# Performance work log

Hardware: AMD Instinct MI355X
Metric: run time of the kernel (lower is better)

The kernel has to match this reference:

```python
import jax, jax.numpy as jnp
import numpy as np

EPS = 1e-5

def _bn_relu(z, gamma, beta):
    # BatchNorm1d (training mode: biased batch stats) + ReLU, per-feature over batch dim
    mean = jnp.mean(z, axis=0)
    var = jnp.var(z, axis=0)  # biased, matches torch BN normalization
    zn = (z - mean) * jax.lax.rsqrt(var + EPS) * gamma + beta
    return jax.nn.relu(zn)


def setup_inputs() -> dict:
    key = jax.random.key(0)
    ks = jax.random.split(key, 16)
    N, D_IN, H, D_OUT = 2097152, 16, 32, 1
    def lin(kw, kb, fan_in, fan_out):
        bound = 1.0 / np.sqrt(fan_in)
        W = jax.random.uniform(kw, (fan_out, fan_in), jnp.float32, -bound, bound)
        b = jax.random.uniform(kb, (fan_out,), jnp.float32, -bound, bound)
        return W, b
    W1, b1 = lin(ks[0], ks[1], D_IN, H)
    W2, b2 = lin(ks[2], ks[3], H, H)
    W3, b3 = lin(ks[4], ks[5], H, H)
    W4, b4 = lin(ks[6], ks[7], H, D_OUT)
    x = jax.random.normal(ks[8], (N, D_IN), jnp.float32)
    return {
        "x": x,
        "W1": W1, "b1": b1, "g1": jnp.ones((H,), jnp.float32), "be1": jnp.zeros((H,), jnp.float32),
        "W2": W2, "b2": b2, "g2": jnp.ones((H,), jnp.float32), "be2": jnp.zeros((H,), jnp.float32),
        "W3": W3, "b3": b3, "g3": jnp.ones((H,), jnp.float32), "be3": jnp.zeros((H,), jnp.float32),
        "W4": W4, "b4": b4,
    }


def reference(x, W1, b1, g1, be1, W2, b2, g2, be2, W3, b3, g3, be3, W4, b4):
    p1 = _bn_relu(x @ W1.T + b1, g1, be1)    # [N, H]
    p2 = _bn_relu(p1 @ W2.T + b2, g2, be2)   # [N, H]
    p3 = _bn_relu(p2 @ W3.T + b3, g3, be3)   # [N, H]
    return p3 @ W4.T + b4                    # [N, 1]
```

## Files before the change

kernel.cpp:

```cpp
#include <hip/hip_runtime.h>

#define EPS 1e-5f
#define NTHR 256
#define NBLK 1024
#define NSLOT 64

typedef __bf16 bf16x8 __attribute__((ext_vector_type(8)));
typedef float f32x16 __attribute__((ext_vector_type(16)));


template<int DEPTH>
__global__ __launch_bounds__(NTHR) void k_fwd(
    const float* __restrict__ x, __bf16* __restrict__ xb,
    const float* __restrict__ W1, const float* __restrict__ b1,
    const float* __restrict__ g1, const float* __restrict__ be1,
    const float* __restrict__ W2, const float* __restrict__ b2,
    const float* __restrict__ g2, const float* __restrict__ be2,
    const float* __restrict__ W3, const float* __restrict__ b3,
    const float* __restrict__ g3, const float* __restrict__ be3,
    const float* __restrict__ W4, const float* __restrict__ b4,
    float* __restrict__ stats, float* __restrict__ out, int N)
{
    constexpr bool STATS = (DEPTH < 4);
    __shared__ float s_stat[3][64];
    __shared__ float s_a[3][32];
    __shared__ float s_e[3][32];
    __shared__ float s_w[NTHR / 64][64];

    const int tid = threadIdx.x;
    const float invN = 1.0f / (float)N;

    if (tid < 64) {
        for (int L = 0; L < DEPTH - 1; ++L) {
            float a = 0.f;
            #pragma unroll 8
            for (int s = 0; s < NSLOT; ++s) a += stats[L * (NSLOT * 64) + s * 64 + tid];
            s_stat[L][tid] = a;
        }
    }
    __syncthreads();
    if (tid < 32) {
        const float* gs[3]  = {g1, g2, g3};
        const float* bes[3] = {be1, be2, be3};
        const float* bs[3]  = {b1, b2, b3};
        for (int L = 0; L < DEPTH - 1; ++L) {
            float mu = s_stat[L][tid] * invN;
            float v  = s_stat[L][32 + tid] * invN - mu * mu;
            float a  = gs[L][tid] * rsqrtf(v + EPS);
            s_a[L][tid] = a;
            s_e[L][tid] = bs[L][tid] - mu + bes[L][tid] / a;
        }
    }
    __syncthreads();

    const int lane = tid & 63;
    const int h = lane >> 5;
    const int ml = lane & 31;

    bf16x8 w1f;
    {
        const float* p = W1 + ml * 16 + h * 8;
        #pragma unroll
        for (int j = 0; j < 8; ++j) w1f[j] = (__bf16)p[j];
    }
    bf16x8 w2f0 = {}, w2f1 = {}, w3f0 = {}, w3f1 = {};
    if (DEPTH >= 2) {
        #pragma unroll
        for (int kh = 0; kh < 2; ++kh)
            #pragma unroll
            for (int j = 0; j < 8; ++j) {
                int pk = (j & 3) + 8 * (j >> 2) + 4 * h + 16 * kh;
                float v = W2[ml * 32 + pk] * s_a[0][pk];
                if (kh == 0) w2f0[j] = (__bf16)v; else w2f1[j] = (__bf16)v;
            }
    }
    if (DEPTH >= 3) {
        #pragma unroll
        for (int kh = 0; kh < 2; ++kh)
            #pragma unroll
            for (int j = 0; j < 8; ++j) {
                int pk = (j & 3) + 8 * (j >> 2) + 4 * h + 16 * kh;
                float v = W3[ml * 32 + pk] * s_a[1][pk];
                if (kh == 0) w3f0[j] = (__bf16)v; else w3f1[j] = (__bf16)v;
            }
    }

    f32x16 c1, c2 = {}, c3 = {};
    float w4c[16];
    #pragma unroll
    for (int i = 0; i < 16; ++i) {
        int p = (i & 3) + 8 * (i >> 2) + 4 * h;
        c1[i] = (DEPTH == 1) ? b1[p] : s_e[0][p];
        if (DEPTH >= 2) c2[i] = (DEPTH == 2) ? b2[p] : s_e[1][p];
        if (DEPTH >= 3) c3[i] = (DEPTH == 3) ? b3[p] : s_e[2][p];
        if (DEPTH == 4) w4c[i] = W4[p] * s_a[2][p]; else w4c[i] = 0.f;
    }
    const float b4v = (DEPTH == 4) ? b4[0] : 0.f;

    const int ntiles = N >> 5;
    const int nwaves = gridDim.x * (NTHR / 64);
    const int gwave  = blockIdx.x * (NTHR / 64) + (tid >> 6);

    float sums[16], sqs[16];
    #pragma unroll
    for (int i = 0; i < 16; ++i) { sums[i] = 0.f; sqs[i] = 0.f; }

    auto tile = [&](int t, bf16x8 xf) {
        f32x16 a1 = __builtin_amdgcn_mfma_f32_32x32x16_bf16(w1f, xf, c1, 0, 0, 0);
        if (DEPTH == 1) {
            #pragma unroll
            for (int i = 0; i < 16; ++i) { sums[i] += a1[i]; sqs[i] = fmaf(a1[i], a1[i], sqs[i]); }
            return;
        }
        bf16x8 qa, qb;
        #pragma unroll
        for (int j = 0; j < 8; ++j) {
            qa[j] = (__bf16)fmaxf(a1[j], 0.f);
            qb[j] = (__bf16)fmaxf(a1[8 + j], 0.f);
        }
        f32x16 a2 = __builtin_amdgcn_mfma_f32_32x32x16_bf16(w2f0, qa, c2, 0, 0, 0);
        a2 = __builtin_amdgcn_mfma_f32_32x32x16_bf16(w2f1, qb, a2, 0, 0, 0);
        if (DEPTH == 2) {
            #pragma unroll
            for (int i = 0; i < 16; ++i) { sums[i] += a2[i]; sqs[i] = fmaf(a2[i], a2[i], sqs[i]); }
            return;
        }
        bf16x8 pa, pb;
        #pragma unroll
        for (int j = 0; j < 8; ++j) {
            pa[j] = (__bf16)fmaxf(a2[j], 0.f);
            pb[j] = (__bf16)fmaxf(a2[8 + j], 0.f);
        }
        f32x16 a3 = __builtin_amdgcn_mfma_f32_32x32x16_bf16(w3f0, pa, c3, 0, 0, 0);
        a3 = __builtin_amdgcn_mfma_f32_32x32x16_bf16(w3f1, pb, a3, 0, 0, 0);
        if (DEPTH == 3) {
            #pragma unroll
            for (int i = 0; i < 16; ++i) { sums[i] += a3[i]; sqs[i] = fmaf(a3[i], a3[i], sqs[i]); }
            return;
        }
        float o = 0.f;
        #pragma unroll
        for (int i = 0; i < 16; ++i) o = fmaf(w4c[i], fmaxf(a3[i], 0.f), o);
        o += __shfl_xor(o, 32);
        if (h == 0) out[(t << 5) + ml] = o + b4v;
    };

    if (DEPTH == 1) {
        for (int t0 = gwave; t0 < ntiles; t0 += 4 * nwaves) {
            float4 u0[4], u1[4];
            #pragma unroll
            for (int k = 0; k < 4; ++k) {
                int t = t0 + k * nwaves;
                if (t < ntiles) {
                    int row = (t << 5) + ml;
                    const float4* xp = (const float4*)(x + (size_t)row * 16 + h * 8);
                    u0[k] = xp[0]; u1[k] = xp[1];
                }
            }
            #pragma unroll
            for (int k = 0; k < 4; ++k) {
                int t = t0 + k * nwaves;
                if (t < ntiles) {
                    bf16x8 xf;
                    xf[0] = (__bf16)u0[k].x; xf[1] = (__bf16)u0[k].y;
                    xf[2] = (__bf16)u0[k].z; xf[3] = (__bf16)u0[k].w;
                    xf[4] = (__bf16)u1[k].x; xf[5] = (__bf16)u1[k].y;
                    xf[6] = (__bf16)u1[k].z; xf[7] = (__bf16)u1[k].w;
                    *(bf16x8*)(xb + ((size_t)t * 64 + lane) * 8) = xf;
                    tile(t, xf);
                }
            }
        }
    } else {
        for (int t0 = gwave; t0 < ntiles; t0 += 8 * nwaves) {
            bf16x8 xf[8];
            #pragma unroll
            for (int k = 0; k < 8; ++k) {
                int t = t0 + k * nwaves;
                if (t < ntiles) xf[k] = *(const bf16x8*)(xb + ((size_t)t * 64 + lane) * 8);
            }
            #pragma unroll
            for (int k = 0; k < 8; ++k) {
                int t = t0 + k * nwaves;
                if (t < ntiles) tile(t, xf[k]);
            }
        }
    }

    if (STATS) {
        const int wid = tid >> 6;
        #pragma unroll
        for (int i = 0; i < 16; ++i) {
            float s = sums[i], q = sqs[i];
            #pragma unroll
            for (int d = 1; d <= 16; d <<= 1) {
                s += __shfl_xor(s, d);
                q += __shfl_xor(q, d);
            }
            if (ml == 0) {
                int p = (i & 3) + 8 * (i >> 2) + 4 * h;
                s_w[wid][p] = s;
                s_w[wid][32 + p] = q;
            }
        }
        __syncthreads();
        if (tid < 64) {
            float a = s_w[0][tid] + s_w[1][tid] + s_w[2][tid] + s_w[3][tid];
            int L = DEPTH - 1;
            atomicAdd(&stats[L * (NSLOT * 64) + (blockIdx.x & (NSLOT - 1)) * 64 + tid], a);
        }
    }
}

extern "C" void kernel_launch(void* const* d_in, const int* in_sizes, int n_in,
                              void* d_out, int out_size, void* d_ws, size_t ws_size,
                              hipStream_t stream) {
    const float* x   = (const float*)d_in[0];
    const float* W1  = (const float*)d_in[1];
    const float* b1  = (const float*)d_in[2];
    const float* g1  = (const float*)d_in[3];
    const float* be1 = (const float*)d_in[4];
    const float* W2  = (const float*)d_in[5];
    const float* b2  = (const float*)d_in[6];
    const float* g2  = (const float*)d_in[7];
    const float* be2 = (const float*)d_in[8];
    const float* W3  = (const float*)d_in[9];
    const float* b3  = (const float*)d_in[10];
    const float* g3  = (const float*)d_in[11];
    const float* be3 = (const float*)d_in[12];
    const float* W4  = (const float*)d_in[13];
    const float* b4  = (const float*)d_in[14];
    float* out = (float*)d_out;
    int N = in_sizes[0] / 16;

    __bf16* xb   = (__bf16*)d_ws;
    float* stats = (float*)((char*)d_ws + (size_t)N * 16 * 2);

    hipMemsetAsync(stats, 0, 3 * NSLOT * 64 * sizeof(float), stream);

    k_fwd<1><<<NBLK, NTHR, 0, stream>>>(x, xb, W1, b1, g1, be1, W2, b2, g2, be2, W3, b3, g3, be3, W4, b4, stats, out, N);
    k_fwd<2><<<NBLK, NTHR, 0, stream>>>(x, xb, W1, b1, g1, be1, W2, b2, g2, be2, W3, b3, g3, be3, W4, b4, stats, out, N);
    k_fwd<3><<<NBLK, NTHR, 0, stream>>>(x, xb, W1, b1, g1, be1, W2, b2, g2, be2, W3, b3, g3, be3, W4, b4, stats, out, N);
    k_fwd<4><<<NBLK, NTHR, 0, stream>>>(x, xb, W1, b1, g1, be1, W2, b2, g2, be2, W3, b3, g3, be3, W4, b4, stats, out, N);
}
```

Baseline: 339.9 us.

## Fuse four BN passes into one persistent kernel with grid barriers

Replaces the four separate depth-templated launches with a single persistent kernel of 512 blocks that runs all four passes, separated by a software grid barrier built on agent-scope atomics. Each wave now owns a contiguous range of tiles and alternates forward and reverse traversal between passes, so recently written bf16 input tiles are more likely to still be in cache. This removes per-launch overhead and the tail idle time between kernels. In exchange it relies on all 512 blocks being co-resident (launch_bounds min 2 blocks per CU) to avoid deadlock, cuts the grid size, and reduces the stat slots to 16, which increases atomic contention.

After: 454.6 us. +33.7%, slower.

```diff
diff --git a/kernel.cpp b/kernel.cpp
--- a/kernel.cpp
+++ b/kernel.cpp
@@ -2,15 +2,14 @@
 
 #define EPS 1e-5f
 #define NTHR 256
-#define NBLK 1024
-#define NSLOT 64
+#define NBLK 512
+#define NSLOT 16
 
 typedef __bf16 bf16x8 __attribute__((ext_vector_type(8)));
 typedef float f32x16 __attribute__((ext_vector_type(16)));
 
 
-template<int DEPTH>
-__global__ __launch_bounds__(NTHR) void k_fwd(
+__global__ __launch_bounds__(NTHR, 2) void k_all(
     const float* __restrict__ x, __bf16* __restrict__ xb,
     const float* __restrict__ W1, const float* __restrict__ b1,
     const float* __restrict__ g1, const float* __restrict__ be1,
@@ -19,175 +18,67 @@
     const float* __restrict__ W3, const float* __restrict__ b3,
     const float* __restrict__ g3, const float* __restrict__ be3,
     const float* __restrict__ W4, const float* __restrict__ b4,
-    float* __restrict__ stats, float* __restrict__ out, int N)
+    float* __restrict__ stats, unsigned* __restrict__ bar,
+    float* __restrict__ out, int N)
 {
-    constexpr bool STATS = (DEPTH < 4);
-    __shared__ float s_stat[3][64];
-    __shared__ float s_a[3][32];
-    __shared__ float s_e[3][32];
+    __shared__ float s_stat[64];
+    __shared__ float s_a[32];
+    __shared__ float s_e[32];
     __shared__ float s_w[NTHR / 64][64];
 
     const int tid = threadIdx.x;
-    const float invN = 1.0f / (float)N;
-
-    if (tid < 64) {
-        for (int L = 0; L < DEPTH - 1; ++L) {
-            float a = 0.f;
-            #pragma unroll 8
-            for (int s = 0; s < NSLOT; ++s) a += stats[L * (NSLOT * 64) + s * 64 + tid];
-            s_stat[L][tid] = a;
-        }
-    }
-    __syncthreads();
-    if (tid < 32) {
-        const float* gs[3]  = {g1, g2, g3};
-        const float* bes[3] = {be1, be2, be3};
-        const float* bs[3]  = {b1, b2, b3};
-        for (int L = 0; L < DEPTH - 1; ++L) {
-            float mu = s_stat[L][tid] * invN;
-            float v  = s_stat[L][32 + tid] * invN - mu * mu;
-            float a  = gs[L][tid] * rsqrtf(v + EPS);
-            s_a[L][tid] = a;
-            s_e[L][tid] = bs[L][tid] - mu + bes[L][tid] / a;
-        }
-    }
-    __syncthreads();
-
     const int lane = tid & 63;
     const int h = lane >> 5;
     const int ml = lane & 31;
-
-    bf16x8 w1f;
-    {
-        const float* p = W1 + ml * 16 + h * 8;
-        #pragma unroll
-        for (int j = 0; j < 8; ++j) w1f[j] = (__bf16)p[j];
-    }
-    bf16x8 w2f0 = {}, w2f1 = {}, w3f0 = {}, w3f1 = {};
-    if (DEPTH >= 2) {
-        #pragma unroll
-        for (int kh = 0; kh < 2; ++kh)
+    const float invN = 1.0f / (float)N;
+
+    const int ntiles = N >> 5;
+    const int nwaves = NBLK * (NTHR / 64);
+    const int gwave  = blockIdx.x * (NTHR / 64) + (tid >> 6);
+    const int tpw    = (ntiles + nwaves - 1) / nwaves;
+    const int t0     = gwave * tpw;
+    const int tend   = (t0 + tpw < ntiles) ? (t0 + tpw) : ntiles;
+    const int cnt    = (tend > t0) ? (tend - t0) : 0;
+
+    auto gbar = [&](unsigned target) {
+        __syncthreads();
+        if (tid == 0) {
+            __threadfence();
+            unsigned old = __hip_atomic_fetch_add(&bar[0], 1u, __ATOMIC_ACQ_REL, __HIP_MEMORY_SCOPE_AGENT);
+            if (old == (unsigned)(NBLK - 1)) {
+                __hip_atomic_store(&bar[0], 0u, __ATOMIC_RELAXED, __HIP_MEMORY_SCOPE_AGENT);
+                __hip_atomic_fetch_add(&bar[1], 1u, __ATOMIC_RELEASE, __HIP_MEMORY_SCOPE_AGENT);
+            } else {
+                while (__hip_atomic_load(&bar[1], __ATOMIC_ACQUIRE, __HIP_MEMORY_SCOPE_AGENT) < target)
+                    __builtin_amdgcn_s_sleep(2);
+            }
+        }
+        __syncthreads();
+    };
+
+    auto derive = [&](int L, const float* g, const float* be, const float* b) {
+        if (tid < 64) {
+            float a = 0.f;
             #pragma unroll
-            for (int j = 0; j < 8; ++j) {
-                int pk = (j & 3) + 8 * (j >> 2) + 4 * h + 16 * kh;
-                float v = W2[ml * 32 + pk] * s_a[0][pk];
-                if (kh == 0) w2f0[j] = (__bf16)v; else w2f1[j] = (__bf16)v;
-            }
-    }
-    if (DEPTH >= 3) {
-        #pragma unroll
-        for (int kh = 0; kh < 2; ++kh)
-            #pragma unroll
-            for (int j = 0; j < 8; ++j) {
-                int pk = (j & 3) + 8 * (j >> 2) + 4 * h + 16 * kh;
-                float v = W3[ml * 32 + pk] * s_a[1][pk];
-                if (kh == 0) w3f0[j] = (__bf16)v; else w3f1[j] = (__bf16)v;
-            }
-    }
-
-    f32x16 c1, c2 = {}, c3 = {};
-    float w4c[16];
-    #pragma unroll
-    for (int i = 0; i < 16; ++i) {
-        int p = (i & 3) + 8 * (i >> 2) + 4 * h;
-        c1[i] = (DEPTH == 1) ? b1[p] : s_e[0][p];
-        if (DEPTH >= 2) c2[i] = (DEPTH == 2) ? b2[p] : s_e[1][p];
-        if (DEPTH >= 3) c3[i] = (DEPTH == 3) ? b3[p] : s_e[2][p];
-        if (DEPTH == 4) w4c[i] = W4[p] * s_a[2][p]; else w4c[i] = 0.f;
-    }
-    const float b4v = (DEPTH == 4) ? b4[0] : 0.f;
-
-    const int ntiles = N >> 5;
-    const int nwaves = gridDim.x * (NTHR / 64);
-    const int gwave  = blockIdx.x * (NTHR / 64) + (tid >> 6);
+            for (int s = 0; s < NSLOT; ++s)
+                a += __hip_atomic_load(&stats[L * (NSLOT * 64) + s * 64 + tid],
+                                       __ATOMIC_RELAXED, __HIP_MEMORY_SCOPE_AGENT);
+            s_stat[tid] = a;
+        }
+        __syncthreads();
+        if (tid < 32) {
+            float mu = s_stat[tid] * invN;
+            float v  = s_stat[32 + tid] * invN - mu * mu;
+            float a  = g[tid] * rsqrtf(v + EPS);
+            s_a[tid] = a;
+            s_e[tid] = b[tid] - mu + be[tid] / a;
+        }
+        __syncthreads();
+    };
 
     float sums[16], sqs[16];
-    #pragma unroll
-    for (int i = 0; i < 16; ++i) { sums[i] = 0.f; sqs[i] = 0.f; }
-
-    auto tile = [&](int t, bf16x8 xf) {
-        f32x16 a1 = __builtin_amdgcn_mfma_f32_32x32x16_bf16(w1f, xf, c1, 0, 0, 0);
-        if (DEPTH == 1) {
-            #pragma unroll
-            for (int i = 0; i < 16; ++i) { sums[i] += a1[i]; sqs[i] = fmaf(a1[i], a1[i], sqs[i]); }
-            return;
-        }
-        bf16x8 qa, qb;
-        #pragma unroll
-        for (int j = 0; j < 8; ++j) {
-            qa[j] = (__bf16)fmaxf(a1[j], 0.f);
-            qb[j] = (__bf16)fmaxf(a1[8 + j], 0.f);
-        }
-        f32x16 a2 = __builtin_amdgcn_mfma_f32_32x32x16_bf16(w2f0, qa, c2, 0, 0, 0);
-        a2 = __builtin_amdgcn_mfma_f32_32x32x16_bf16(w2f1, qb, a2, 0, 0, 0);
-        if (DEPTH == 2) {
-            #pragma unroll
-            for (int i = 0; i < 16; ++i) { sums[i] += a2[i]; sqs[i] = fmaf(a2[i], a2[i], sqs[i]); }
-            return;
-        }
-        bf16x8 pa, pb;
-        #pragma unroll
-        for (int j = 0; j < 8; ++j) {
-            pa[j] = (__bf16)fmaxf(a2[j], 0.f);
-            pb[j] = (__bf16)fmaxf(a2[8 + j], 0.f);
-        }
-        f32x16 a3 = __builtin_amdgcn_mfma_f32_32x32x16_bf16(w3f0, pa, c3, 0, 0, 0);
-        a3 = __builtin_amdgcn_mfma_f32_32x32x16_bf16(w3f1, pb, a3, 0, 0, 0);
-        if (DEPTH == 3) {
-            #pragma unroll
-            for (int i = 0; i < 16; ++i) { sums[i] += a3[i]; sqs[i] = fmaf(a3[i], a3[i], sqs[i]); }
-            return;
-        }
-        float o = 0.f;
-        #pragma unroll
-        for (int i = 0; i < 16; ++i) o = fmaf(w4c[i], fmaxf(a3[i], 0.f), o);
-        o += __shfl_xor(o, 32);
-        if (h == 0) out[(t << 5) + ml] = o + b4v;
-    };
-
-    if (DEPTH == 1) {
-        for (int t0 = gwave; t0 < ntiles; t0 += 4 * nwaves) {
-            float4 u0[4], u1[4];
-            #pragma unroll
-            for (int k = 0; k < 4; ++k) {
-                int t = t0 + k * nwaves;
-                if (t < ntiles) {
-                    int row = (t << 5) + ml;
-                    const float4* xp = (const float4*)(x + (size_t)row * 16 + h * 8);
-                    u0[k] = xp[0]; u1[k] = xp[1];
-                }
-            }
-            #pragma unroll
-            for (int k = 0; k < 4; ++k) {
-                int t = t0 + k * nwaves;
-                if (t < ntiles) {
-                    bf16x8 xf;
-                    xf[0] = (__bf16)u0[k].x; xf[1] = (__bf16)u0[k].y;
-                    xf[2] = (__bf16)u0[k].z; xf[3] = (__bf16)u0[k].w;
-                    xf[4] = (__bf16)u1[k].x; xf[5] = (__bf16)u1[k].y;
-                    xf[6] = (__bf16)u1[k].z; xf[7] = (__bf16)u1[k].w;
-                    *(bf16x8*)(xb + ((size_t)t * 64 + lane) * 8) = xf;
-                    tile(t, xf);
-                }
-            }
-        }
-    } else {
-        for (int t0 = gwave; t0 < ntiles; t0 += 8 * nwaves) {
-            bf16x8 xf[8];
-            #pragma unroll
-            for (int k = 0; k < 8; ++k) {
-                int t = t0 + k * nwaves;
-                if (t < ntiles) xf[k] = *(const bf16x8*)(xb + ((size_t)t * 64 + lane) * 8);
-            }
-            #pragma unroll
-            for (int k = 0; k < 8; ++k) {
-                int t = t0 + k * nwaves;
-                if (t < ntiles) tile(t, xf[k]);
-            }
-        }
-    }
-
-    if (STATS) {
+
+    auto flush_stats = [&](int L) {
         const int wid = tid >> 6;
         #pragma unroll
         for (int i = 0; i < 16; ++i) {
@@ -206,8 +97,223 @@
         __syncthreads();
         if (tid < 64) {
             float a = s_w[0][tid] + s_w[1][tid] + s_w[2][tid] + s_w[3][tid];
-            int L = DEPTH - 1;
             atomicAdd(&stats[L * (NSLOT * 64) + (blockIdx.x & (NSLOT - 1)) * 64 + tid], a);
+        }
+    };
+
+    bf16x8 w1f;
+    {
+        const float* p = W1 + ml * 16 + h * 8;
+        #pragma unroll
+        for (int j = 0; j < 8; ++j) w1f[j] = (__bf16)p[j];
+    }
+    f32x16 c1;
+    #pragma unroll
+    for (int i = 0; i < 16; ++i) {
+        int p = (i & 3) + 8 * (i >> 2) + 4 * h;
+        c1[i] = b1[p];
+    }
+
+    #pragma unroll
+    for (int i = 0; i < 16; ++i) { sums[i] = 0.f; sqs[i] = 0.f; }
+    for (int i0 = 0; i0 < cnt; i0 += 4) {
+        float4 u0[4], u1[4];
+        #pragma unroll
+        for (int k = 0; k < 4; ++k) {
+            int i = i0 + k;
+            if (i < cnt) {
+                int row = ((t0 + i) << 5) + ml;
+                const float4* xp = (const float4*)(x + (size_t)row * 16 + h * 8);
+                u0[k] = xp[0]; u1[k] = xp[1];
+            }
+        }
+        #pragma unroll
+        for (int k = 0; k < 4; ++k) {
+            int i = i0 + k;
+            if (i < cnt) {
+                int t = t0 + i;
+                bf16x8 xf;
+                xf[0] = (__bf16)u0[k].x; xf[1] = (__bf16)u0[k].y;
+                xf[2] = (__bf16)u0[k].z; xf[3] = (__bf16)u0[k].w;
+                xf[4] = (__bf16)u1[k].x; xf[5] = (__bf16)u1[k].y;
+                xf[6] = (__bf16)u1[k].z; xf[7] = (__bf16)u1[k].w;
+                *(bf16x8*)(xb + ((size_t)t * 64 + lane) * 8) = xf;
+                f32x16 a1 = __builtin_amdgcn_mfma_f32_32x32x16_bf16(w1f, xf, c1, 0, 0, 0);
+                #pragma unroll
+                for (int q = 0; q < 16; ++q) { sums[q] += a1[q]; sqs[q] = fmaf(a1[q], a1[q], sqs[q]); }
+            }
+        }
+    }
+    flush_stats(0);
+    gbar(1);
+
+    derive(0, g1, be1, b1);
+    #pragma unroll
+    for (int i = 0; i < 16; ++i) {
+        int p = (i & 3) + 8 * (i >> 2) + 4 * h;
+        c1[i] = s_e[p];
+    }
+    bf16x8 w2f0, w2f1;
+    #pragma unroll
+    for (int kh = 0; kh < 2; ++kh)
+        #pragma unroll
+        for (int j = 0; j < 8; ++j) {
+            int pk = (j & 3) + 8 * (j >> 2) + 4 * h + 16 * kh;
+            float v = W2[ml * 32 + pk] * s_a[pk];
+            if (kh == 0) w2f0[j] = (__bf16)v; else w2f1[j] = (__bf16)v;
+        }
+    f32x16 c2;
+    #pragma unroll
+    for (int i = 0; i < 16; ++i) {
+        int p = (i & 3) + 8 * (i >> 2) + 4 * h;
+        c2[i] = b2[p];
+    }
+    #pragma unroll
+    for (int i = 0; i < 16; ++i) { sums[i] = 0.f; sqs[i] = 0.f; }
+    for (int i0 = 0; i0 < cnt; i0 += 4) {
+        bf16x8 xf[4];
+        #pragma unroll
+        for (int k = 0; k < 4; ++k) {
+            int i = i0 + k;
+            if (i < cnt) {
+                int t = tend - 1 - i;
+                xf[k] = *(const bf16x8*)(xb + ((size_t)t * 64 + lane) * 8);
+            }
+        }
+        #pragma unroll
+        for (int k = 0; k < 4; ++k) {
+            int i = i0 + k;
+            if (i < cnt) {
+                f32x16 a1 = __builtin_amdgcn_mfma_f32_32x32x16_bf16(w1f, xf[k], c1, 0, 0, 0);
+                bf16x8 qa, qb;
+                #pragma unroll
+                for (int j = 0; j < 8; ++j) {
+                    qa[j] = (__bf16)fmaxf(a1[j], 0.f);
+                    qb[j] = (__bf16)fmaxf(a1[8 + j], 0.f);
+                }
+                f32x16 a2 = __builtin_amdgcn_mfma_f32_32x32x16_bf16(w2f0, qa, c2, 0, 0, 0);
+                a2 = __builtin_amdgcn_mfma_f32_32x32x16_bf16(w2f1, qb, a2, 0, 0, 0);
+                #pragma unroll
+                for (int q = 0; q < 16; ++q) { sums[q] += a2[q]; sqs[q] = fmaf(a2[q], a2[q], sqs[q]); }
+            }
+        }
+    }
+    flush_stats(1);
+    gbar(2);
+
+    derive(1, g2, be2, b2);
+    #pragma unroll
+    for (int i = 0; i < 16; ++i) {
+        int p = (i & 3) + 8 * (i >> 2) + 4 * h;
+        c2[i] = s_e[p];
+    }
+    bf16x8 w3f0, w3f1;
+    #pragma unroll
+    for (int kh = 0; kh < 2; ++kh)
+        #pragma unroll
+        for (int j = 0; j < 8; ++j) {
+            int pk = (j & 3) + 8 * (j >> 2) + 4 * h + 16 * kh;
+            float v = W3[ml * 32 + pk] * s_a[pk];
+            if (kh == 0) w3f0[j] = (__bf16)v; else w3f1[j] = (__bf16)v;
+        }
+    f32x16 c3;
+    #pragma unroll
+    for (int i = 0; i < 16; ++i) {
+        int p = (i & 3) + 8 * (i >> 2) + 4 * h;
+        c3[i] = b3[p];
+    }
+    #pragma unroll
+    for (int i = 0; i < 16; ++i) { sums[i] = 0.f; sqs[i] = 0.f; }
+    for (int i0 = 0; i0 < cnt; i0 += 4) {
+        bf16x8 xf[4];
+        #pragma unroll
+        for (int k = 0; k < 4; ++k) {
+            int i = i0 + k;
+            if (i < cnt) {
+                int t = t0 + i;
+                xf[k] = *(const bf16x8*)(xb + ((size_t)t * 64 + lane) * 8);
+            }
+        }
+        #pragma unroll
+        for (int k = 0; k < 4; ++k) {
+            int i = i0 + k;
+            if (i < cnt) {
+                f32x16 a1 = __builtin_amdgcn_mfma_f32_32x32x16_bf16(w1f, xf[k], c1, 0, 0, 0);
+                bf16x8 qa, qb;
+                #pragma unroll
+                for (int j = 0; j < 8; ++j) {
+                    qa[j] = (__bf16)fmaxf(a1[j], 0.f);
+                    qb[j] = (__bf16)fmaxf(a1[8 + j], 0.f);
+                }
+                f32x16 a2 = __builtin_amdgcn_mfma_f32_32x32x16_bf16(w2f0, qa, c2, 0, 0, 0);
+                a2 = __builtin_amdgcn_mfma_f32_32x32x16_bf16(w2f1, qb, a2, 0, 0, 0);
+                bf16x8 pa, pb;
+                #pragma unroll
+                for (int j = 0; j < 8; ++j) {
+                    pa[j] = (__bf16)fmaxf(a2[j], 0.f);
+                    pb[j] = (__bf16)fmaxf(a2[8 + j], 0.f);
+                }
+                f32x16 a3 = __builtin_amdgcn_mfma_f32_32x32x16_bf16(w3f0, pa, c3, 0, 0, 0);
+                a3 = __builtin_amdgcn_mfma_f32_32x32x16_bf16(w3f1, pb, a3, 0, 0, 0);
+                #pragma unroll
+                for (int q = 0; q < 16; ++q) { sums[q] += a3[q]; sqs[q] = fmaf(a3[q], a3[q], sqs[q]); }
+            }
+        }
+    }
+    flush_stats(2);
+    gbar(3);
+
+    derive(2, g3, be3, b3);
+    #pragma unroll
+    for (int i = 0; i < 16; ++i) {
+        int p = (i & 3) + 8 * (i >> 2) + 4 * h;
+        c3[i] = s_e[p];
+    }
+    float w4c[16];
+    #pragma unroll
+    for (int i = 0; i < 16; ++i) {
+        int p = (i & 3) + 8 * (i >> 2) + 4 * h;
+        w4c[i] = W4[p] * s_a[p];
+    }
+    const float b4v = b4[0];
+    for (int i0 = 0; i0 < cnt; i0 += 4) {
+        bf16x8 xf[4];
+        #pragma unroll
+        for (int k = 0; k < 4; ++k) {
+            int i = i0 + k;
+            if (i < cnt) {
+                int t = tend - 1 - i;
+                xf[k] = *(const bf16x8*)(xb + ((size_t)t * 64 + lane) * 8);
+            }
+        }
+        #pragma unroll
+        for (int k = 0; k < 4; ++k) {
+            int i = i0 + k;
+            if (i < cnt) {
+                int t = tend - 1 - i;
+                f32x16 a1 = __builtin_amdgcn_mfma_f32_32x32x16_bf16(w1f, xf[k], c1, 0, 0, 0);
+                bf16x8 qa, qb;
+                #pragma unroll
+                for (int j = 0; j < 8; ++j) {
+                    qa[j] = (__bf16)fmaxf(a1[j], 0.f);
+                    qb[j] = (__bf16)fmaxf(a1[8 + j], 0.f);
+                }
+                f32x16 a2 = __builtin_amdgcn_mfma_f32_32x32x16_bf16(w2f0, qa, c2, 0, 0, 0);
+                a2 = __builtin_amdgcn_mfma_f32_32x32x16_bf16(w2f1, qb, a2, 0, 0, 0);
+                bf16x8 pa, pb;
+                #pragma unroll
+                for (int j = 0; j < 8; ++j) {
+                    pa[j] = (__bf16)fmaxf(a2[j], 0.f);
+                    pb[j] = (__bf16)fmaxf(a2[8 + j], 0.f);
+                }
+                f32x16 a3 = __builtin_amdgcn_mfma_f32_32x32x16_bf16(w3f0, pa, c3, 0, 0, 0);
+                a3 = __builtin_amdgcn_mfma_f32_32x32x16_bf16(w3f1, pb, a3, 0, 0, 0);
+                float o = 0.f;
+                #pragma unroll
+                for (int q = 0; q < 16; ++q) o = fmaf(w4c[q], fmaxf(a3[q], 0.f), o);
+                o += __shfl_xor(o, 32);
+                if (h == 0) out[(t << 5) + ml] = o + b4v;
+            }
         }
     }
 }
@@ -233,13 +339,12 @@
     float* out = (float*)d_out;
     int N = in_sizes[0] / 16;
 
-    __bf16* xb   = (__bf16*)d_ws;
-    float* stats = (float*)((char*)d_ws + (size_t)N * 16 * 2);
-
-    hipMemsetAsync(stats, 0, 3 * NSLOT * 64 * sizeof(float), stream);
-
-    k_fwd<1><<<NBLK, NTHR, 0, stream>>>(x, xb, W1, b1, g1, be1, W2, b2, g2, be2, W3, b3, g3, be3, W4, b4, stats, out, N);
-    k_fwd<2><<<NBLK, NTHR, 0, stream>>>(x, xb, W1, b1, g1, be1, W2, b2, g2, be2, W3, b3, g3, be3, W4, b4, stats, out, N);
-    k_fwd<3><<<NBLK, NTHR, 0, stream>>>(x, xb, W1, b1, g1, be1, W2, b2, g2, be2, W3, b3, g3, be3, W4, b4, stats, out, N);
-    k_fwd<4><<<NBLK, NTHR, 0, stream>>>(x, xb, W1, b1, g1, be1, W2, b2, g2, be2, W3, b3, g3, be3, W4, b4, stats, out, N);
+    __bf16* xb    = (__bf16*)d_ws;
+    float* stats  = (float*)((char*)d_ws + (size_t)N * 16 * 2);
+    unsigned* bar = (unsigned*)((char*)stats + 3 * NSLOT * 64 * sizeof(float));
+
+    hipMemsetAsync(stats, 0, 3 * NSLOT * 64 * sizeof(float) + 64, stream);
+
+    k_all<<<NBLK, NTHR, 0, stream>>>(x, xb, W1, b1, g1, be1, W2, b2, g2, be2,
+                                     W3, b3, g3, be3, W4, b4, stats, bar, out, N);
 }
```
